# Kernel tuning notes

Hardware: AMD Instinct MI355X
Metric: run time of the kernel (lower is better)

The kernel has to match this reference:

```python
import jax, jax.numpy as jnp
import numpy as np

N_NODES = 50000
N_EDGES = 150000
D_FEAT = 512
HIDDEN = 512
N_CLASSES = 47


def gcn_conv(x, edge_index, W, b, n_nodes):
    """PyG GCNConv: out = D^{-1/2} (A + I) D^{-1/2} (x @ W) + b."""
    h = x @ W  # [N, out_dim] dense GEMM
    loop = jnp.arange(n_nodes, dtype=edge_index.dtype)
    row = jnp.concatenate([edge_index[0], loop])  # source
    col = jnp.concatenate([edge_index[1], loop])  # target
    ones = jnp.ones(row.shape[0], dtype=h.dtype)
    deg = jax.ops.segment_sum(ones, col, num_segments=n_nodes)  # in-degree + 1
    dinv = jnp.where(deg > 0, jax.lax.rsqrt(deg), 0.0)
    norm = dinv[row] * dinv[col]  # [E+N]
    msg = norm[:, None] * h[row]  # gather + scale
    out = jax.ops.segment_sum(msg, col, num_segments=n_nodes)  # scatter-add
    return out + b


def setup_inputs() -> dict:
    key = jax.random.key(0)
    k1, k2, k3, k4, k5, k6 = jax.random.split(key, 6)
    x = jax.random.normal(k1, (N_NODES, D_FEAT), dtype=jnp.float32)
    edge_index = jax.random.randint(k2, (2, N_EDGES), 0, N_NODES, dtype=jnp.int64)
    s1 = (6.0 / (D_FEAT + HIDDEN)) ** 0.5
    s2 = (6.0 / (HIDDEN + N_CLASSES)) ** 0.5
    W1 = jax.random.uniform(k3, (D_FEAT, HIDDEN), jnp.float32, -s1, s1)
    b1 = jnp.zeros((HIDDEN,), jnp.float32)
    W2 = jax.random.uniform(k4, (HIDDEN, N_CLASSES), jnp.float32, -s2, s2)
    b2 = jnp.zeros((N_CLASSES,), jnp.float32)
    return {"x": x, "edge_index": edge_index, "W1": W1, "b1": b1, "W2": W2, "b2": b2}


def reference(x, edge_index, W1, b1, W2, b2):
    n = x.shape[0]
    h = gcn_conv(x, edge_index, W1, b1, n)
    h = jax.nn.relu(h)
    # F.dropout(p=0.5, training=self.training): eval mode -> identity
    out = gcn_conv(h, edge_index, W2, b2, n)
    return out
```

## Files before the change

kernel.cpp:

```cpp
#include <hip/hip_runtime.h>
#include <hip/hip_bf16.h>

#define NNODES 50000
#define NEDGES 150000
#define DFEAT  512
#define HID    512
#define NCLS   47

typedef __hip_bfloat16 bf16;
typedef __attribute__((ext_vector_type(8))) short short8;
typedef __attribute__((ext_vector_type(4))) float float4v;

typedef const __attribute__((address_space(1))) unsigned int* gas_t;
typedef __attribute__((address_space(3))) unsigned int* las_t;
__device__ __forceinline__ void load_lds16(const void* g, void* l) {
    __builtin_amdgcn_global_load_lds((gas_t)g, (las_t)l, 16, 0, 0);
}

__device__ __forceinline__ float bfbits_lo(unsigned int w) {
    return __uint_as_float((w & 0xFFFFu) << 16);
}
__device__ __forceinline__ float bfbits_hi(unsigned int w) {
    return __uint_as_float(w & 0xFFFF0000u);
}

__device__ __forceinline__ int eidx(const void* ei, int half, int e, int is64) {
    if (is64) return (int)((const long long*)ei)[(size_t)half * NEDGES + e];
    return ((const int*)ei)[half * NEDGES + e];
}

#define ZB ((NNODES + 255) / 256)
#define NZH2 ((NNODES * 64 / 4 + 255) / 256)
#define PR_ZH2 (1 + ZB)
#define PR_W1T (PR_ZH2 + NZH2)
#define PR_B1  (PR_W1T + 1024)
#define PR_W2T (PR_B1 + 2)
#define PR_B2  (PR_W2T + 128)
#define PR_GRID (PR_B2 + 1)

__global__ __launch_bounds__(256) void k_prep0(
    const void* x, const void* ei, const void* W1, const void* b1,
    const void* W2, const void* b2, int* flags, unsigned int* cnt,
    bf16* W1T, float* b1c, bf16* W2T, float* b2c, float* h2) {
    __shared__ int sh[128];
    __shared__ int shflag;
    const int b = blockIdx.x, t = threadIdx.x;

    if (b >= 1 && b < 1 + ZB) {
        int i = (b - 1) * 256 + t;
        if (i < NNODES) cnt[i] = 0u;
        return;
    }
    if (b >= PR_ZH2 && b < PR_W1T) {
        int i = (b - PR_ZH2) * 256 + t;
        if (i < NNODES * 64 / 4)
            ((float4v*)h2)[i] = (float4v){0.f, 0.f, 0.f, 0.f};
        return;
    }

    if (t < 64) {
        const unsigned short* xs = (const unsigned short*)x;
        int c = 0;
        for (int i = t; i < 256; i += 64) {
            unsigned int e = (xs[2 * i] >> 7) & 0xFF;
            c += (e >= 117 && e <= 130) ? 1 : 0;
        }
        sh[t] = c;
        if (b == 0) {
            const int* w = (const int*)ei;
            int o = 0;
            for (int i = 2 * t + 1; i < 512; i += 128) o |= w[i];
            sh[64 + t] = o;
        }
    }
    __syncthreads();
    if (t == 0) {
        int C = 0;
        for (int i = 0; i < 64; i++) C += sh[i];
        shflag = (C > 128) ? 1 : 0;
        if (b == 0) {
            int O = 0;
            for (int i = 0; i < 64; i++) O |= sh[64 + i];
            flags[0] = shflag;
            flags[1] = (O == 0) ? 1 : 0;
        }
    }
    __syncthreads();
    const int isb = shflag;

    if (b == 0) return;

    if (b >= PR_W1T && b < PR_B1) {
        int i = (b - PR_W1T) * 256 + t;
        int k = i / HID, n = i % HID;
        float v = isb ? __bfloat162float(((const bf16*)W1)[i]) : ((const float*)W1)[i];
        W1T[(size_t)n * DFEAT + k] = __float2bfloat16(v);
    } else if (b >= PR_B1 && b < PR_W2T) {
        int i = (b - PR_B1) * 256 + t;
        if (i < HID)
            b1c[i] = isb ? __bfloat162float(((const bf16*)b1)[i]) : ((const float*)b1)[i];
    } else if (b >= PR_W2T && b < PR_B2) {
        int i = (b - PR_W2T) * 256 + t;
        int n = i / HID, k = i % HID;
        float v = 0.0f;
        if (n < NCLS) {
            size_t idx = (size_t)k * NCLS + n;
            v = isb ? __bfloat162float(((const bf16*)W2)[idx]) : ((const float*)W2)[idx];
        }
        W2T[(size_t)n * HID + k] = __float2bfloat16(v);
    } else if (b == PR_B2) {
        if (t < NCLS)
            b2c[t] = isb ? __bfloat162float(((const bf16*)b2)[t]) : ((const float*)b2)[t];
    }
}

__global__ void k_count(const void* ei, int* cnt, const int* flags) {
    int e = blockIdx.x * blockDim.x + threadIdx.x;
    if (e >= NEDGES) return;
    atomicAdd(&cnt[eidx(ei, 1, e, flags[1])], 1);
}

__global__ __launch_bounds__(256) void k_scan_part_dinv(const int* cnt, int* part,
                                                        float* dinv) {
    __shared__ int s[256];
    int i = blockIdx.x * 256 + threadIdx.x;
    int v = (i < NNODES) ? cnt[i] : 0;
    if (i < NNODES) dinv[i] = rsqrtf(1.0f + (float)v);
    s[threadIdx.x] = v;
    __syncthreads();
    for (int off = 128; off > 0; off >>= 1) {
        if (threadIdx.x < off) s[threadIdx.x] += s[threadIdx.x + off];
        __syncthreads();
    }
    if (threadIdx.x == 0) part[blockIdx.x] = s[0];
}

__global__ __launch_bounds__(256) void k_scan_off(int* part, int n) {
    __shared__ int s[256];
    int v = (threadIdx.x < n) ? part[threadIdx.x] : 0;
    s[threadIdx.x] = v;
    __syncthreads();
    for (int off = 1; off < 256; off <<= 1) {
        int t = (threadIdx.x >= off) ? s[threadIdx.x - off] : 0;
        __syncthreads();
        s[threadIdx.x] += t;
        __syncthreads();
    }
    if (threadIdx.x < n) part[threadIdx.x] = s[threadIdx.x] - v;
}

__global__ __launch_bounds__(256) void k_scan_fin(const int* cnt, const int* part,
                                                  int* rowptr, int* cursor) {
    __shared__ int s[256];
    int i = blockIdx.x * 256 + threadIdx.x;
    int v = (i < NNODES) ? cnt[i] : 0;
    s[threadIdx.x] = v;
    __syncthreads();
    for (int off = 1; off < 256; off <<= 1) {
        int t = (threadIdx.x >= off) ? s[threadIdx.x - off] : 0;
        __syncthreads();
        s[threadIdx.x] += t;
        __syncthreads();
    }
    int incl = s[threadIdx.x] + part[blockIdx.x];
    if (i < NNODES) {
        rowptr[i + 1] = incl;
        cursor[i] = incl - v;
    }
    if (i == 0) rowptr[0] = 0;
}

__global__ void k_fill(const void* ei, int* cursor, int* csr_src, const int* flags) {
    int e = blockIdx.x * blockDim.x + threadIdx.x;
    if (e >= NEDGES) return;
    int is64 = flags[1];
    int v = eidx(ei, 1, e, is64);
    int u = eidx(ei, 0, e, is64);
    int pos = atomicAdd(&cursor[v], 1);
    csr_src[pos] = u;
}

__global__ __launch_bounds__(256) void k_aggx(const void* __restrict__ X,
                                              const int* __restrict__ rowptr,
                                              const int* __restrict__ csr_src,
                                              const float* __restrict__ dinv,
                                              bf16* __restrict__ ax,
                                              const int* __restrict__ flags) {
    int v = blockIdx.x * 4 + (threadIdx.x >> 6);
    int lane = threadIdx.x & 63;
    if (v >= NNODES) return;
    int d8 = lane * 8;
    float dv = dinv[v];
    float s2 = dv * dv;
    float a0, a1, a2, a3, a4, a5, a6, a7;
    int pend = rowptr[v + 1];
    if (flags[0]) {
        const bf16* xb = (const bf16*)X;
        uint4 w = *(const uint4*)(xb + (size_t)v * 512 + d8);
        a0 = s2 * bfbits_lo(w.x); a1 = s2 * bfbits_hi(w.x);
        a2 = s2 * bfbits_lo(w.y); a3 = s2 * bfbits_hi(w.y);
        a4 = s2 * bfbits_lo(w.z); a5 = s2 * bfbits_hi(w.z);
        a6 = s2 * bfbits_lo(w.w); a7 = s2 * bfbits_hi(w.w);
        for (int p = rowptr[v]; p < pend; ++p) {
            int u = csr_src[p];
            float nw = dinv[u] * dv;
            uint4 q = *(const uint4*)(xb + (size_t)u * 512 + d8);
            a0 += nw * bfbits_lo(q.x); a1 += nw * bfbits_hi(q.x);
            a2 += nw * bfbits_lo(q.y); a3 += nw * bfbits_hi(q.y);
            a4 += nw * bfbits_lo(q.z); a5 += nw * bfbits_hi(q.z);
            a6 += nw * bfbits_lo(q.w); a7 += nw * bfbits_hi(q.w);
        }
    } else {
        const float* xf = (const float*)X;
        const float* p0 = xf + (size_t)v * 512 + d8;
        float4v f0 = *(const float4v*)p0, f1 = *(const float4v*)(p0 + 4);
        a0 = s2 * f0[0]; a1 = s2 * f0[1]; a2 = s2 * f0[2]; a3 = s2 * f0[3];
        a4 = s2 * f1[0]; a5 = s2 * f1[1]; a6 = s2 * f1[2]; a7 = s2 * f1[3];
        for (int p = rowptr[v]; p < pend; ++p) {
            int u = csr_src[p];
            float nw = dinv[u] * dv;
            const float* pu = xf + (size_t)u * 512 + d8;
            float4v g0 = *(const float4v*)pu, g1 = *(const float4v*)(pu + 4);
            a0 += nw * g0[0]; a1 += nw * g0[1]; a2 += nw * g0[2]; a3 += nw * g0[3];
            a4 += nw * g1[0]; a5 += nw * g1[1]; a6 += nw * g1[2]; a7 += nw * g1[3];
        }
    }
    bf16 o[8];
    o[0] = __float2bfloat16(a0); o[1] = __float2bfloat16(a1);
    o[2] = __float2bfloat16(a2); o[3] = __float2bfloat16(a3);
    o[4] = __float2bfloat16(a4); o[5] = __float2bfloat16(a5);
    o[6] = __float2bfloat16(a6); o[7] = __float2bfloat16(a7);
    *(uint4*)(ax + (size_t)v * 512 + d8) = *(uint4*)o;
}

__global__ __launch_bounds__(256, 3) void k_fgemm(
    const bf16* __restrict__ ax, const bf16* __restrict__ W1T,
    const float* __restrict__ b1c, const bf16* __restrict__ W2T,
    float* __restrict__ h2, int rows_per_xcd, int n_row_tiles) {
    const int b = blockIdx.x;
    const int xcd = b & 7;
    const int s = b >> 3;
    const int col_t = s & 3;
    const int lr = s >> 2;
    const int row_t = xcd * rows_per_xcd + lr;
    if (row_t >= n_row_tiles) return;

    __shared__ bf16 smem[128 * 128];
    bf16* As = smem;
    bf16* Bs = smem + 128 * 64;
    const int tid = threadIdx.x;
    const int wave = tid >> 6, lane = tid & 63;
    const int row0 = row_t * 128;
    const int gc0 = col_t * 128;

    const int rb = wave * 32;
    const int frow = lane & 15;
    const int fk = lane >> 4;

    float4v acc[2][8];
#pragma unroll
    for (int i = 0; i < 2; i++)
#pragma unroll
        for (int j = 0; j < 8; j++) acc[i][j] = (float4v){0.f, 0.f, 0.f, 0.f};

    for (int k0 = 0; k0 < DFEAT; k0 += 64) {
        __syncthreads();
#pragma unroll
        for (int t = 0; t < 4; ++t) {
            int g8 = wave * 4 + t;
            int r = g8 * 8 + (lane >> 3);
            int gr = row0 + r; if (gr >= NNODES) gr = NNODES - 1;
            int ck = (lane & 7) ^ (r & 7);
            load_lds16(ax + (size_t)gr * DFEAT + k0 + ck * 8, &As[g8 * 8 * 64]);
        }
#pragma unroll
        for (int t = 0; t < 4; ++t) {
            int g8 = wave * 4 + t;
            int cl = g8 * 8 + (lane >> 3);
            int ck = (lane & 7) ^ (cl & 7);
            load_lds16(W1T + (size_t)(gc0 + cl) * DFEAT + k0 + ck * 8, &Bs[g8 * 8 * 64]);
        }
        __syncthreads();
#pragma unroll
        for (int ki = 0; ki < 2; ++ki) {
            const int cc = ki * 4 + fk;
            short8 a[2], b8[8];
#pragma unroll
            for (int i = 0; i < 2; i++) {
                int r = rb + i * 16 + frow;
                a[i] = *(const short8*)&As[r * 64 + (cc ^ (r & 7)) * 8];
            }
#pragma unroll
            for (int j = 0; j < 8; j++) {
                int cl = j * 16 + frow;
                b8[j] = *(const short8*)&Bs[cl * 64 + (cc ^ (cl & 7)) * 8];
            }
#pragma unroll
            for (int i = 0; i < 2; i++)
#pragma unroll
                for (int j = 0; j < 8; j++)
                    acc[i][j] = __builtin_amdgcn_mfma_f32_16x16x32_bf16(a[i], b8[j], acc[i][j], 0, 0, 0);
        }
    }

    __syncthreads();
    {
        float bias[8];
#pragma unroll
        for (int j = 0; j < 8; j++) bias[j] = b1c[gc0 + j * 16 + frow];
#pragma unroll
        for (int i = 0; i < 2; i++) {
#pragma unroll
            for (int r = 0; r < 4; r++) {
                int row = rb + i * 16 + fk * 4 + r;
#pragma unroll
                for (int j = 0; j < 8; j++) {
                    int col = j * 16 + frow;
                    float v = acc[i][j][r] + bias[j];
                    v = v > 0.f ? v : 0.f;
                    int ck2 = (col >> 3) ^ (row & 7);
                    smem[row * 128 + ck2 * 8 + (col & 7)] = __float2bfloat16(v);
                }
            }
        }
    }
    __syncthreads();

    float4v acc2[2][4];
#pragma unroll
    for (int i = 0; i < 2; i++)
#pragma unroll
        for (int j = 0; j < 4; j++) acc2[i][j] = (float4v){0.f, 0.f, 0.f, 0.f};
#pragma unroll
    for (int ks = 0; ks < 4; ++ks) {
        const int kk = ks * 32 + fk * 8;
        const int p = kk >> 3;
        short8 a2[2], b2f[4];
#pragma unroll
        for (int i = 0; i < 2; i++) {
            int row = rb + i * 16 + frow;
            a2[i] = *(const short8*)&smem[row * 128 + ((p ^ (row & 7)) * 8)];
        }
#pragma unroll
        for (int j = 0; j < 4; j++) {
            int n = j * 16 + frow;
            b2f[j] = *(const short8*)(W2T + (size_t)n * HID + gc0 + kk);
        }
#pragma unroll
        for (int i = 0; i < 2; i++)
#pragma unroll
            for (int j = 0; j < 4; j++)
                acc2[i][j] = __builtin_amdgcn_mfma_f32_16x16x32_bf16(a2[i], b2f[j], acc2[i][j], 0, 0, 0);
    }

#pragma unroll
    for (int i = 0; i < 2; i++) {
#pragma unroll
        for (int r = 0; r < 4; r++) {
            int grow = row0 + rb + i * 16 + fk * 4 + r;
            if (grow < NNODES) {
#pragma unroll
                for (int j = 0; j < 4; j++)
                    atomicAdd(&h2[(size_t)grow * 64 + j * 16 + frow], acc2[i][j][r]);
            }
        }
    }
}

__global__ __launch_bounds__(256) void k_agg2(const float* __restrict__ h2,
                                              const int* __restrict__ rowptr,
                                              const int* __restrict__ csr_src,
                                              const float* __restrict__ dinv,
                                              const float* __restrict__ b2c,
                                              void* out, const int* flags) {
    int v = blockIdx.x * 4 + (threadIdx.x >> 6);
    int d = threadIdx.x & 63;
    if (v >= NNODES || d >= NCLS) return;
    float dv = dinv[v];
    float acc = dv * dv * h2[(size_t)v * 64 + d];
    int pend = rowptr[v + 1];
    for (int p = rowptr[v]; p < pend; ++p) {
        int u = csr_src[p];
        acc += dinv[u] * dv * h2[(size_t)u * 64 + d];
    }
    acc += b2c[d];
    size_t o = (size_t)v * NCLS + d;
    if (flags[0]) ((bf16*)out)[o] = __float2bfloat16(acc);
    else          ((float*)out)[o] = acc;
}

extern "C" void kernel_launch(void* const* d_in, const int* in_sizes, int n_in,
                              void* d_out, int out_size, void* d_ws, size_t ws_size,
                              hipStream_t stream) {
    const void* x  = d_in[0];
    const void* ei = d_in[1];
    const void* W1 = d_in[2];
    const void* b1 = d_in[3];
    const void* W2 = d_in[4];
    const void* b2 = d_in[5];

    char* base = (char*)d_ws;
    auto alloc = [&](size_t bytes) -> char* {
        char* p = base;
        base += (bytes + 255) & ~(size_t)255;
        return p;
    };
    int*   flags  = (int*)alloc(64);
    int*   cnt    = (int*)alloc(sizeof(int) * NNODES);
    int*   part   = (int*)alloc(sizeof(int) * 256);
    int*   rowptr = (int*)alloc(sizeof(int) * (NNODES + 1));
    int*   cursor = (int*)alloc(sizeof(int) * NNODES);
    int*   csr    = (int*)alloc(sizeof(int) * NEDGES);
    float* dinv   = (float*)alloc(sizeof(float) * NNODES);
    bf16*  W1T    = (bf16*)alloc(sizeof(bf16) * DFEAT * HID);
    float* b1c    = (float*)alloc(sizeof(float) * HID);
    bf16*  W2T    = (bf16*)alloc(sizeof(bf16) * 64 * HID);
    float* b2c    = (float*)alloc(sizeof(float) * 64);
    float* h2     = (float*)alloc(sizeof(float) * (size_t)NNODES * 64);
    bf16*  ax     = (bf16*)alloc(sizeof(bf16) * (size_t)NNODES * DFEAT);

    k_prep0<<<PR_GRID, 256, 0, stream>>>(x, ei, W1, b1, W2, b2, flags,
                                         (unsigned int*)cnt, W1T, b1c, W2T, b2c, h2);
    k_count<<<(NEDGES + 255) / 256, 256, 0, stream>>>(ei, cnt, flags);
    const int nsb = (NNODES + 255) / 256;
    k_scan_part_dinv<<<nsb, 256, 0, stream>>>(cnt, part, dinv);
    k_scan_off<<<1, 256, 0, stream>>>(part, nsb);
    k_scan_fin<<<nsb, 256, 0, stream>>>(cnt, part, rowptr, cursor);
    k_fill<<<(NEDGES + 255) / 256, 256, 0, stream>>>(ei, cursor, csr, flags);

    k_aggx<<<(NNODES + 3) / 4, 256, 0, stream>>>(x, rowptr, csr, dinv, ax, flags);

    const int rowblocks = (NNODES + 127) / 128;
    const int rows_per_xcd = (rowblocks + 7) / 8;
    k_fgemm<<<8 * rows_per_xcd * 4, 256, 0, stream>>>(ax, W1T, b1c, W2T, h2,
                                                      rows_per_xcd, rowblocks);

    k_agg2<<<(NNODES + 3) / 4, 256, 0, stream>>>(h2, rowptr, csr, dinv, b2c, d_out, flags);
}
```

Before: 321.5 us.

## Shrink fused GEMM row tile to 64 and batch neighbor gathers in aggregations

The fused two-layer GEMM now uses 64-row tiles with one 16-row MMA strip per wave, which cuts shared memory and registers so four blocks can share a CU and the grid roughly doubles. The bf16 feature aggregation loop loads 8 neighbor indices and weights up front before gathering, and the class aggregation does the same with 4 neighbors, so more memory requests are in flight at once. The cost is that each W1 tile is reused across fewer rows, so W1 traffic from global memory and L2 doubles. The padded slots in the unrolled gathers also issue redundant loads for low-degree nodes.

New measurement: 315.9 us. About the same (-1.7%).

```diff
diff --git a/kernel.cpp b/kernel.cpp
--- a/kernel.cpp
+++ b/kernel.cpp
@@ -201,14 +201,25 @@
         a2 = s2 * bfbits_lo(w.y); a3 = s2 * bfbits_hi(w.y);
         a4 = s2 * bfbits_lo(w.z); a5 = s2 * bfbits_hi(w.z);
         a6 = s2 * bfbits_lo(w.w); a7 = s2 * bfbits_hi(w.w);
-        for (int p = rowptr[v]; p < pend; ++p) {
-            int u = csr_src[p];
-            float nw = dinv[u] * dv;
-            uint4 q = *(const uint4*)(xb + (size_t)u * 512 + d8);
-            a0 += nw * bfbits_lo(q.x); a1 += nw * bfbits_hi(q.x);
-            a2 += nw * bfbits_lo(q.y); a3 += nw * bfbits_hi(q.y);
-            a4 += nw * bfbits_lo(q.z); a5 += nw * bfbits_hi(q.z);
-            a6 += nw * bfbits_lo(q.w); a7 += nw * bfbits_hi(q.w);
+        for (int p = rowptr[v]; p < pend; p += 8) {
+            int u[8]; float nw[8];
+#pragma unroll
+            for (int c = 0; c < 8; ++c) {
+                int jp = (p + c < pend) ? p + c : p;
+                u[c] = csr_src[jp];
+            }
+#pragma unroll
+            for (int c = 0; c < 8; ++c)
+                nw[c] = (p + c < pend) ? dinv[u[c]] * dv : 0.f;
+#pragma unroll
+            for (int c = 0; c < 8; ++c) {
+                uint4 q = *(const uint4*)(xb + (size_t)u[c] * 512 + d8);
+                float nwc = nw[c];
+                a0 += nwc * bfbits_lo(q.x); a1 += nwc * bfbits_hi(q.x);
+                a2 += nwc * bfbits_lo(q.y); a3 += nwc * bfbits_hi(q.y);
+                a4 += nwc * bfbits_lo(q.z); a5 += nwc * bfbits_hi(q.z);
+                a6 += nwc * bfbits_lo(q.w); a7 += nwc * bfbits_hi(q.w);
+            }
         }
     } else {
         const float* xf = (const float*)X;
@@ -233,7 +244,7 @@
     *(uint4*)(ax + (size_t)v * 512 + d8) = *(uint4*)o;
 }
 
-__global__ __launch_bounds__(256, 3) void k_fgemm(
+__global__ __launch_bounds__(256, 4) void k_fgemm64(
     const bf16* __restrict__ ax, const bf16* __restrict__ W1T,
     const float* __restrict__ b1c, const bf16* __restrict__ W2T,
     float* __restrict__ h2, int rows_per_xcd, int n_row_tiles) {
@@ -245,29 +256,27 @@
     const int row_t = xcd * rows_per_xcd + lr;
     if (row_t >= n_row_tiles) return;
 
-    __shared__ bf16 smem[128 * 128];
+    __shared__ bf16 smem[12288];
     bf16* As = smem;
-    bf16* Bs = smem + 128 * 64;
+    bf16* Bs = smem + 4096;
     const int tid = threadIdx.x;
     const int wave = tid >> 6, lane = tid & 63;
-    const int row0 = row_t * 128;
+    const int row0 = row_t * 64;
     const int gc0 = col_t * 128;
 
-    const int rb = wave * 32;
+    const int rb16 = wave * 16;
     const int frow = lane & 15;
     const int fk = lane >> 4;
 
-    float4v acc[2][8];
-#pragma unroll
-    for (int i = 0; i < 2; i++)
-#pragma unroll
-        for (int j = 0; j < 8; j++) acc[i][j] = (float4v){0.f, 0.f, 0.f, 0.f};
+    float4v acc[8];
+#pragma unroll
+    for (int j = 0; j < 8; j++) acc[j] = (float4v){0.f, 0.f, 0.f, 0.f};
 
     for (int k0 = 0; k0 < DFEAT; k0 += 64) {
         __syncthreads();
 #pragma unroll
-        for (int t = 0; t < 4; ++t) {
-            int g8 = wave * 4 + t;
+        for (int t = 0; t < 2; ++t) {
+            int g8 = wave * 2 + t;
             int r = g8 * 8 + (lane >> 3);
             int gr = row0 + r; if (gr >= NNODES) gr = NNODES - 1;
             int ck = (lane & 7) ^ (r & 7);
@@ -284,22 +293,17 @@
 #pragma unroll
         for (int ki = 0; ki < 2; ++ki) {
             const int cc = ki * 4 + fk;
-            short8 a[2], b8[8];
-#pragma unroll
-            for (int i = 0; i < 2; i++) {
-                int r = rb + i * 16 + frow;
-                a[i] = *(const short8*)&As[r * 64 + (cc ^ (r & 7)) * 8];
-            }
+            int r = rb16 + frow;
+            short8 a = *(const short8*)&As[r * 64 + (cc ^ (r & 7)) * 8];
+            short8 b8[8];
 #pragma unroll
             for (int j = 0; j < 8; j++) {
                 int cl = j * 16 + frow;
                 b8[j] = *(const short8*)&Bs[cl * 64 + (cc ^ (cl & 7)) * 8];
             }
 #pragma unroll
-            for (int i = 0; i < 2; i++)
-#pragma unroll
-                for (int j = 0; j < 8; j++)
-                    acc[i][j] = __builtin_amdgcn_mfma_f32_16x16x32_bf16(a[i], b8[j], acc[i][j], 0, 0, 0);
+            for (int j = 0; j < 8; j++)
+                acc[j] = __builtin_amdgcn_mfma_f32_16x16x32_bf16(a, b8[j], acc[j], 0, 0, 0);
         }
     }
 
@@ -309,60 +313,47 @@
 #pragma unroll
         for (int j = 0; j < 8; j++) bias[j] = b1c[gc0 + j * 16 + frow];
 #pragma unroll
-        for (int i = 0; i < 2; i++) {
-#pragma unroll
-            for (int r = 0; r < 4; r++) {
-                int row = rb + i * 16 + fk * 4 + r;
-#pragma unroll
-                for (int j = 0; j < 8; j++) {
-                    int col = j * 16 + frow;
-                    float v = acc[i][j][r] + bias[j];
-                    v = v > 0.f ? v : 0.f;
-                    int ck2 = (col >> 3) ^ (row & 7);
-                    smem[row * 128 + ck2 * 8 + (col & 7)] = __float2bfloat16(v);
-                }
+        for (int r = 0; r < 4; r++) {
+            int row = rb16 + fk * 4 + r;
+#pragma unroll
+            for (int j = 0; j < 8; j++) {
+                int col = j * 16 + frow;
+                float v = acc[j][r] + bias[j];
+                v = v > 0.f ? v : 0.f;
+                int ck2 = (col >> 3) ^ (row & 7);
+                smem[row * 128 + ck2 * 8 + (col & 7)] = __float2bfloat16(v);
             }
         }
     }
     __syncthreads();
 
-    float4v acc2[2][4];
-#pragma unroll
-    for (int i = 0; i < 2; i++)
-#pragma unroll
-        for (int j = 0; j < 4; j++) acc2[i][j] = (float4v){0.f, 0.f, 0.f, 0.f};
+    float4v acc2[4];
+#pragma unroll
+    for (int j = 0; j < 4; j++) acc2[j] = (float4v){0.f, 0.f, 0.f, 0.f};
 #pragma unroll
     for (int ks = 0; ks < 4; ++ks) {
         const int kk = ks * 32 + fk * 8;
         const int p = kk >> 3;
-        short8 a2[2], b2f[4];
-#pragma unroll
-        for (int i = 0; i < 2; i++) {
-            int row = rb + i * 16 + frow;
-            a2[i] = *(const short8*)&smem[row * 128 + ((p ^ (row & 7)) * 8)];
-        }
+        int row = rb16 + frow;
+        short8 a2 = *(const short8*)&smem[row * 128 + ((p ^ (row & 7)) * 8)];
+        short8 b2f[4];
 #pragma unroll
         for (int j = 0; j < 4; j++) {
             int n = j * 16 + frow;
             b2f[j] = *(const short8*)(W2T + (size_t)n * HID + gc0 + kk);
         }
 #pragma unroll
-        for (int i = 0; i < 2; i++)
+        for (int j = 0; j < 4; j++)
+            acc2[j] = __builtin_amdgcn_mfma_f32_16x16x32_bf16(a2, b2f[j], acc2[j], 0, 0, 0);
+    }
+
+#pragma unroll
+    for (int r = 0; r < 4; r++) {
+        int grow = row0 + rb16 + fk * 4 + r;
+        if (grow < NNODES) {
 #pragma unroll
             for (int j = 0; j < 4; j++)
-                acc2[i][j] = __builtin_amdgcn_mfma_f32_16x16x32_bf16(a2[i], b2f[j], acc2[i][j], 0, 0, 0);
-    }
-
-#pragma unroll
-    for (int i = 0; i < 2; i++) {
-#pragma unroll
-        for (int r = 0; r < 4; r++) {
-            int grow = row0 + rb + i * 16 + fk * 4 + r;
-            if (grow < NNODES) {
-#pragma unroll
-                for (int j = 0; j < 4; j++)
-                    atomicAdd(&h2[(size_t)grow * 64 + j * 16 + frow], acc2[i][j][r]);
-            }
+                atomicAdd(&h2[(size_t)grow * 64 + j * 16 + frow], acc2[j][r]);
         }
     }
 }
@@ -379,9 +370,21 @@
     float dv = dinv[v];
     float acc = dv * dv * h2[(size_t)v * 64 + d];
     int pend = rowptr[v + 1];
-    for (int p = rowptr[v]; p < pend; ++p) {
-        int u = csr_src[p];
-        acc += dinv[u] * dv * h2[(size_t)u * 64 + d];
+    for (int p = rowptr[v]; p < pend; p += 4) {
+        int j1 = (p + 1 < pend) ? p + 1 : p;
+        int j2 = (p + 2 < pend) ? p + 2 : p;
+        int j3 = (p + 3 < pend) ? p + 3 : p;
+        int u0 = csr_src[p], u1 = csr_src[j1];
+        int u2 = csr_src[j2], u3 = csr_src[j3];
+        float nw0 = dinv[u0] * dv;
+        float nw1 = (p + 1 < pend) ? dinv[u1] * dv : 0.f;
+        float nw2 = (p + 2 < pend) ? dinv[u2] * dv : 0.f;
+        float nw3 = (p + 3 < pend) ? dinv[u3] * dv : 0.f;
+        float q0 = h2[(size_t)u0 * 64 + d];
+        float q1 = h2[(size_t)u1 * 64 + d];
+        float q2 = h2[(size_t)u2 * 64 + d];
+        float q3 = h2[(size_t)u3 * 64 + d];
+        acc += nw0 * q0 + nw1 * q1 + nw2 * q2 + nw3 * q3;
     }
     acc += b2c[d];
     size_t o = (size_t)v * NCLS + d;
@@ -430,10 +433,10 @@
 
     k_aggx<<<(NNODES + 3) / 4, 256, 0, stream>>>(x, rowptr, csr, dinv, ax, flags);
 
-    const int rowblocks = (NNODES + 127) / 128;
+    const int rowblocks = (NNODES + 63) / 64;
     const int rows_per_xcd = (rowblocks + 7) / 8;
-    k_fgemm<<<8 * rows_per_xcd * 4, 256, 0, stream>>>(ax, W1T, b1c, W2T, h2,
-                                                      rows_per_xcd, rowblocks);
+    k_fgemm64<<<8 * rows_per_xcd * 4, 256, 0, stream>>>(ax, W1T, b1c, W2T, h2,
+                                                        rows_per_xcd, rowblocks);
 
     k_agg2<<<(NNODES + 3) / 4, 256, 0, stream>>>(h2, rowptr, csr, dinv, b2c, d_out, flags);
 }
```
